# Optimization experiments

Hardware: AMD Instinct MI355X
Metric: run time of the kernel (lower is better)

Reference implementation:

```python
import jax, jax.numpy as jnp
import numpy as np


def _gat_layer(x, W, att_l, att_r, b, src, dst, num_nodes, heads, out_feat, concat):
    # x: [N, in], W: [in, H*F]
    xl = (x @ W).reshape(num_nodes, heads, out_feat)          # [N, H, F]
    a_l = jnp.sum(xl * att_l, axis=2)                          # [N, H]
    a_r = jnp.sum(xl * att_r, axis=2)                          # [N, H]
    # edge scores: alpha_j (source, att_l) + alpha_i (target, att_r)
    e = a_l[src] + a_r[dst]                                    # [E, H]
    e = jax.nn.leaky_relu(e, 0.2)
    # segment softmax over destination-node neighborhoods
    e_max = jax.ops.segment_max(e, dst, num_segments=num_nodes)
    e_exp = jnp.exp(e - e_max[dst])
    denom = jax.ops.segment_sum(e_exp, dst, num_segments=num_nodes)
    alpha = e_exp / (denom[dst] + 1e-16)                       # [E, H]
    # weighted gather + scatter-add aggregation
    msg = alpha[:, :, None] * xl[src]                          # [E, H, F]
    out = jax.ops.segment_sum(msg, dst, num_segments=num_nodes)  # [N, H, F]
    if concat:
        out = out.reshape(num_nodes, heads * out_feat)
    else:
        out = out.mean(axis=1)                                 # [N, F]
    return out + b


def setup_inputs() -> dict:
    key = jax.random.key(0)
    ks = jax.random.split(key, 8)
    N, E = 50000, 800000
    in_dim, hidden, out_dim, H = 128, 8, 64, 8
    x = jax.random.normal(ks[0], (N, in_dim), dtype=jnp.float32)
    edge_index = jax.random.randint(ks[1], (2, E), 0, N, dtype=jnp.int64)
    s = 0.1
    return {
        "x": x,
        "edge_index": edge_index,
        "W1": jax.random.normal(ks[2], (in_dim, hidden * H), dtype=jnp.float32) * s,
        "att_l1": jax.random.normal(ks[3], (1, H, hidden), dtype=jnp.float32) * s,
        "att_r1": jax.random.normal(ks[4], (1, H, hidden), dtype=jnp.float32) * s,
        "b1": jnp.zeros((hidden * H,), dtype=jnp.float32),
        "W2": jax.random.normal(ks[5], (hidden * H, out_dim * H), dtype=jnp.float32) * s,
        "att_l2": jax.random.normal(ks[6], (1, H, out_dim), dtype=jnp.float32) * s,
        "att_r2": jax.random.normal(ks[7], (1, H, out_dim), dtype=jnp.float32) * s,
        "b2": jnp.zeros((1, out_dim), dtype=jnp.float32),
    }


def reference(x, edge_index, W1, att_l1, att_r1, b1, W2, att_l2, att_r2, b2):
    N = x.shape[0]
    H = att_l1.shape[1]
    src, dst = edge_index[0], edge_index[1]
    h = _gat_layer(x, W1, att_l1, att_r1, b1, src, dst, N, H, att_l1.shape[2], concat=True)
    h = jax.nn.relu(h)
    out = _gat_layer(h, W2, att_l2, att_r2, b2, src, dst, N, H, att_l2.shape[2], concat=False)
    return out
```

## Files before the change

### kernel.cpp

```cpp
#include <hip/hip_runtime.h>
#include <stdint.h>

#define NT 256
#define CHUNK 4096
#define BSHIFT 8

typedef __attribute__((ext_vector_type(8))) short bf16x8;
typedef __attribute__((ext_vector_type(4))) float f32x4;

__device__ __forceinline__ float lrelu(float x) { return x > 0.f ? x : 0.2f * x; }

__device__ __forceinline__ float b2f(unsigned short u) {
  union { unsigned int i; float f; } v; v.i = ((unsigned int)u) << 16; return v.f;
}
__device__ __forceinline__ unsigned short f2b(float f) {
  unsigned int u = __float_as_uint(f);
  return (unsigned short)((u + 0x7fffu + ((u >> 16) & 1u)) >> 16);
}

__global__ void detect_kernel(const int* __restrict__ ei, int* __restrict__ flag, int twoE) {
  __shared__ int any;
  if (threadIdx.x == 0) any = 0;
  __syncthreads();
  int n = twoE < 4096 ? twoE : 4096;
  for (int i = threadIdx.x * 2 + 1; i < n; i += 2 * NT)
    if (ei[i] != 0) any = 1;
  __syncthreads();
  if (threadIdx.x == 0) *flag = any;
}

__global__ void cvtbin_kernel(const void* __restrict__ ei, const int* __restrict__ flag,
                              int* __restrict__ edges, int* __restrict__ blkcnt,
                              int E, int nblk, int nbk) {
  __shared__ int cnt[256];
  int b = blockIdx.x;
  for (int i = threadIdx.x; i < nbk; i += NT) cnt[i] = 0;
  __syncthreads();
  int beg = b * CHUNK;
  int end = beg + CHUNK < E ? beg + CHUNK : E;
  bool is32 = (*flag != 0);
  for (int i = beg + threadIdx.x; i < end; i += NT) {
    int s, d;
    if (is32) { s = ((const int*)ei)[i]; d = ((const int*)ei)[E + i]; }
    else      { s = (int)((const long long*)ei)[i]; d = (int)((const long long*)ei)[E + i]; }
    edges[i] = s;
    edges[E + i] = d;
    atomicAdd(&cnt[d >> BSHIFT], 1);
  }
  __syncthreads();
  for (int i = threadIdx.x; i < nbk; i += NT) blkcnt[i * nblk + b] = cnt[i];
}

__global__ void zero2_kernel(int* __restrict__ a, int* __restrict__ b, int n) {
  int i = blockIdx.x * NT + threadIdx.x;
  if (i < n) { a[i] = 0; b[i] = 0; }
}

__global__ void scan1_kernel(const int* __restrict__ in, int* __restrict__ bsum, int n) {
  __shared__ int sm[NT];
  int idx = blockIdx.x * NT + threadIdx.x;
  sm[threadIdx.x] = (idx < n) ? in[idx] : 0;
  __syncthreads();
  for (int s = NT / 2; s > 0; s >>= 1) {
    if (threadIdx.x < s) sm[threadIdx.x] += sm[threadIdx.x + s];
    __syncthreads();
  }
  if (threadIdx.x == 0) bsum[blockIdx.x] = sm[0];
}

__global__ void scan2_kernel(const int* __restrict__ bsum, int* __restrict__ boff, int SB) {
  __shared__ int sm[NT];
  int t = threadIdx.x;
  int v = (t < SB) ? bsum[t] : 0;
  sm[t] = v;
  __syncthreads();
  for (int s = 1; s < NT; s <<= 1) {
    int add = (t >= s) ? sm[t - s] : 0;
    __syncthreads();
    sm[t] += add;
    __syncthreads();
  }
  if (t < SB) boff[t] = sm[t] - v;
}

__global__ void scan3_kernel(const int* __restrict__ in, const int* __restrict__ boff,
                             int* __restrict__ out, int n) {
  __shared__ int sm[NT];
  int idx = blockIdx.x * NT + threadIdx.x;
  int v = (idx < n) ? in[idx] : 0;
  sm[threadIdx.x] = v;
  __syncthreads();
  for (int s = 1; s < NT; s <<= 1) {
    int add = (threadIdx.x >= s) ? sm[threadIdx.x - s] : 0;
    __syncthreads();
    sm[threadIdx.x] += add;
    __syncthreads();
  }
  if (idx <= n) out[idx] = boff[blockIdx.x] + sm[threadIdx.x] - v;
}

__global__ void binwrite_kernel(const int* __restrict__ src, const int* __restrict__ dst,
                                const int* __restrict__ base, long long* __restrict__ binned,
                                int E, int nblk, int nbk) {
  __shared__ int cnt[256];
  int b = blockIdx.x;
  for (int i = threadIdx.x; i < nbk; i += NT) cnt[i] = base[i * nblk + b];
  __syncthreads();
  int beg = b * CHUNK;
  int end = beg + CHUNK < E ? beg + CHUNK : E;
  for (int i = beg + threadIdx.x; i < end; i += NT) {
    int d = dst[i];
    int pos = atomicAdd(&cnt[d >> BSHIFT], 1);
    binned[pos] = ((long long)d << 32) | (unsigned int)src[i];
  }
}

__global__ void deghist_kernel(const long long* __restrict__ binned, int* __restrict__ deg, int E) {
  int e = blockIdx.x * NT + threadIdx.x;
  if (e < E) atomicAdd(&deg[(int)(binned[e] >> 32)], 1);
}

__global__ void scatter2_kernel(const long long* __restrict__ binned, const int* __restrict__ rowptr,
                                int* __restrict__ cursor, int* __restrict__ csr_src, int E) {
  int e = blockIdx.x * NT + threadIdx.x;
  if (e >= E) return;
  long long v = binned[e];
  int d = (int)(v >> 32);
  int s = (int)(v & 0xffffffffLL);
  int pos = rowptr[d] + atomicAdd(&cursor[d], 1);
  csr_src[pos] = s;
}

__global__ void foldB1_kernel(const float* __restrict__ W1, unsigned short* __restrict__ W1pack) {
  int idx = blockIdx.x * NT + threadIdx.x;
  if (idx >= 128 * 64) return;
  int j = idx & 7;
  int lane = (idx >> 3) & 63;
  int ctchunk = idx >> 9;
  int ct = ctchunk & 3;
  int chunk = ctchunk >> 2;
  int k = chunk * 32 + ((lane >> 4) << 3) + j;
  int col = ct * 16 + (lane & 15);
  W1pack[idx] = f2b(W1[k * 64 + col]);
}

__global__ void __launch_bounds__(NT)
gemm1_mfma_kernel(const float* __restrict__ x, const unsigned short* __restrict__ W1pack,
                  const float* __restrict__ attl, const float* __restrict__ attr,
                  unsigned short* __restrict__ xl1b, float* __restrict__ a1, int N) {
  int w = threadIdx.x >> 6;
  int lane = threadIdx.x & 63;
  int colb = lane & 15;
  int rgrp = lane >> 4;
  int row0w = blockIdx.x * 64 + w * 16;
  int arow = row0w + colb;
  if (arow >= N) arow = N - 1;
  const float* ap = x + (size_t)arow * 128 + (rgrp << 3);

  f32x4 acc[4];
#pragma unroll
  for (int ct = 0; ct < 4; ++ct) { acc[ct][0] = 0.f; acc[ct][1] = 0.f; acc[ct][2] = 0.f; acc[ct][3] = 0.f; }

#pragma unroll
  for (int chunk = 0; chunk < 4; ++chunk) {
    float4 v0 = *(const float4*)(ap + chunk * 32);
    float4 v1 = *(const float4*)(ap + chunk * 32 + 4);
    bf16x8 a;
    a[0] = (short)f2b(v0.x); a[1] = (short)f2b(v0.y);
    a[2] = (short)f2b(v0.z); a[3] = (short)f2b(v0.w);
    a[4] = (short)f2b(v1.x); a[5] = (short)f2b(v1.y);
    a[6] = (short)f2b(v1.z); a[7] = (short)f2b(v1.w);
    const unsigned short* bp = W1pack + ((size_t)chunk * 4 * 64 + lane) * 8;
#pragma unroll
    for (int ct = 0; ct < 4; ++ct) {
      bf16x8 b = *(const bf16x8*)(bp + (size_t)ct * 64 * 8);
      acc[ct] = __builtin_amdgcn_mfma_f32_16x16x32_bf16(a, b, acc[ct], 0, 0, 0);
    }
  }

#pragma unroll
  for (int ct = 0; ct < 4; ++ct) {
    float attlc = attl[ct * 16 + colb];
    float attrc = attr[ct * 16 + colb];
    int h = ct * 2 + (colb >> 3);
#pragma unroll
    for (int r = 0; r < 4; ++r) {
      int n = row0w + rgrp * 4 + r;
      float v = acc[ct][r];
      if (n < N) xl1b[(size_t)n * 64 + ct * 16 + colb] = f2b(v);
      float pl = v * attlc;
      float pr = v * attrc;
      pl += __shfl_xor(pl, 1, 64); pr += __shfl_xor(pr, 1, 64);
      pl += __shfl_xor(pl, 2, 64); pr += __shfl_xor(pr, 2, 64);
      pl += __shfl_xor(pl, 4, 64); pr += __shfl_xor(pr, 4, 64);
      if ((lane & 7) == 0 && n < N) {
        a1[n * 16 + h] = pl;
        a1[n * 16 + 8 + h] = pr;
      }
    }
  }
}

__global__ void foldw_kernel(const float* __restrict__ W2, const float* __restrict__ attl2,
                             const float* __restrict__ attr2, float* __restrict__ wl,
                             float* __restrict__ wr) {
  int t = threadIdx.x;
  int k = t >> 3, h = t & 7;
  float sl = 0.f, sr = 0.f;
  for (int f = 0; f < 64; ++f) {
    float w = W2[k * 512 + h * 64 + f];
    sl += w * attl2[h * 64 + f];
    sr += w * attr2[h * 64 + f];
  }
  wl[k * 8 + h] = sl;
  wr[k * 8 + h] = sr;
}

__global__ void foldB_kernel(const float* __restrict__ W2, unsigned short* __restrict__ Bpack) {
  int idx = blockIdx.x * NT + threadIdx.x;
  if (idx >= 512 * 64) return;
  int j = idx & 7;
  int lane = (idx >> 3) & 63;
  int ctchunk = idx >> 9;
  int ct = ctchunk & 3;
  int chunk = ctchunk >> 2;
  int hk = chunk * 32 + ((lane >> 4) << 3) + j;
  int h = hk >> 6, kk = hk & 63;
  int f = ct * 16 + (lane & 15);
  Bpack[idx] = f2b(W2[kk * 512 + h * 64 + f] * 0.125f);
}

__global__ void __launch_bounds__(NT)
node_aggr1_kernel(const int* __restrict__ rowptr, const int* __restrict__ csr_src,
                  const float* __restrict__ a1, const unsigned short* __restrict__ xl1b,
                  const float* __restrict__ b1, unsigned short* __restrict__ hrb, int N) {
  __shared__ float ps[4][64][8];
  __shared__ int ss[4][64];
  int w = threadIdx.x >> 6;
  int n = blockIdx.x * 4 + w;
  if (n >= N) return;
  int lane = threadIdx.x & 63;
  int hstage = lane & 7;
  int j8 = lane >> 3;
  int hown = lane >> 3;
  int base = rowptr[n];
  int deg = rowptr[n + 1] - base;

  float arh = a1[n * 16 + 8 + hstage];
  const unsigned short* xp = xl1b + lane;
  float acc = 0.f, dn = 0.f;

  for (int j0 = 0; j0 < deg; j0 += 64) {
    int cnt = deg - j0; if (cnt > 64) cnt = 64;
    if (lane < cnt) ss[w][lane] = csr_src[base + j0 + lane];
    asm volatile("s_waitcnt lgkmcnt(0)" ::: "memory");
    for (int jj = 0; jj < cnt; jj += 8) {
      int j = jj + j8;
      if (j < cnt) {
        int s = ss[w][j];
        float p = __expf(lrelu(a1[(unsigned)s * 16 + hstage] + arh));
        ps[w][j][hstage] = p;
      }
    }
    asm volatile("s_waitcnt lgkmcnt(0)" ::: "memory");
    int j = 0;
    for (; j + 4 <= cnt; j += 4) {
      int s0 = ss[w][j+0], s1 = ss[w][j+1], s2 = ss[w][j+2], s3 = ss[w][j+3];
      float p0 = ps[w][j+0][hown], p1 = ps[w][j+1][hown];
      float p2 = ps[w][j+2][hown], p3 = ps[w][j+3][hown];
      float v0 = b2f(xp[(unsigned)s0 * 64]), v1 = b2f(xp[(unsigned)s1 * 64]);
      float v2 = b2f(xp[(unsigned)s2 * 64]), v3 = b2f(xp[(unsigned)s3 * 64]);
      dn += (p0 + p1) + (p2 + p3);
      acc += p0 * v0 + p1 * v1 + p2 * v2 + p3 * v3;
    }
    for (; j < cnt; ++j) {
      int s = ss[w][j];
      float p = ps[w][j][hown];
      dn += p;
      acc += p * b2f(xp[(unsigned)s * 64]);
    }
  }
  acc = acc / (dn + 1e-16f);
  float hv = fmaxf(acc + b1[lane], 0.f);
  hrb[(size_t)n * 64 + lane] = f2b(hv);
}

#define A2N 256
__global__ void __launch_bounds__(NT)
a2dots_kernel(const unsigned short* __restrict__ hrb, const float* __restrict__ wl,
              const float* __restrict__ wr, float* __restrict__ a2, int N) {
  __shared__ unsigned short hs[A2N][65];
  __shared__ float wls[64 * 8], wrs[64 * 8];
  int tid = threadIdx.x;
  int n0 = blockIdx.x * A2N;
  for (int i = tid; i < 512; i += NT) { wls[i] = wl[i]; wrs[i] = wr[i]; }
  for (int i = tid; i < A2N * 8; i += NT) {
    int r = i >> 3, seg = i & 7;
    int n = n0 + r;
    uint4 v = make_uint4(0, 0, 0, 0);
    if (n < N) v = *(const uint4*)&hrb[(size_t)n * 64 + seg * 8];
    int c = seg * 8;
    hs[r][c + 0] = (unsigned short)(v.x);
    hs[r][c + 1] = (unsigned short)(v.x >> 16);
    hs[r][c + 2] = (unsigned short)(v.y);
    hs[r][c + 3] = (unsigned short)(v.y >> 16);
    hs[r][c + 4] = (unsigned short)(v.z);
    hs[r][c + 5] = (unsigned short)(v.z >> 16);
    hs[r][c + 6] = (unsigned short)(v.w);
    hs[r][c + 7] = (unsigned short)(v.w >> 16);
  }
  __syncthreads();
  float tl[8], tr[8];
#pragma unroll
  for (int h = 0; h < 8; ++h) { tl[h] = 0.f; tr[h] = 0.f; }
#pragma unroll 4
  for (int k = 0; k < 64; ++k) {
    float hv = b2f(hs[tid][k]);
    float4 l0 = *(const float4*)&wls[k * 8];
    float4 l1 = *(const float4*)&wls[k * 8 + 4];
    float4 r0 = *(const float4*)&wrs[k * 8];
    float4 r1 = *(const float4*)&wrs[k * 8 + 4];
    tl[0] += hv * l0.x; tl[1] += hv * l0.y; tl[2] += hv * l0.z; tl[3] += hv * l0.w;
    tl[4] += hv * l1.x; tl[5] += hv * l1.y; tl[6] += hv * l1.z; tl[7] += hv * l1.w;
    tr[0] += hv * r0.x; tr[1] += hv * r0.y; tr[2] += hv * r0.z; tr[3] += hv * r0.w;
    tr[4] += hv * r1.x; tr[5] += hv * r1.y; tr[6] += hv * r1.z; tr[7] += hv * r1.w;
  }
  int n = n0 + tid;
  if (n < N) {
    *(float4*)&a2[n * 16 + 0]  = make_float4(tl[0], tl[1], tl[2], tl[3]);
    *(float4*)&a2[n * 16 + 4]  = make_float4(tl[4], tl[5], tl[6], tl[7]);
    *(float4*)&a2[n * 16 + 8]  = make_float4(tr[0], tr[1], tr[2], tr[3]);
    *(float4*)&a2[n * 16 + 12] = make_float4(tr[4], tr[5], tr[6], tr[7]);
  }
}

__global__ void __launch_bounds__(NT)
node_aggr2_fused_kernel(const int* __restrict__ rowptr, const int* __restrict__ csr_src,
                        const float* __restrict__ a2, const unsigned short* __restrict__ hrb,
                        const unsigned short* __restrict__ Bpack, const float* __restrict__ b2,
                        float* __restrict__ out, int N) {
  __shared__ float ps[4][64][8];
  __shared__ int ss[4][64];
  __shared__ unsigned short gs[16][520];
  int w = threadIdx.x >> 6;
  int lane = threadIdx.x & 63;
  int hstage = lane & 7;
  int j8 = lane >> 3;

  for (int nr = 0; nr < 4; ++nr) {
    int row = w * 4 + nr;
    int n = blockIdx.x * 16 + row;
    if (n < N) {
      int base = rowptr[n];
      int deg = rowptr[n + 1] - base;
      float arh = a2[n * 16 + 8 + hstage];
      const unsigned short* hp = hrb + lane;
      float acc[8] = {0.f, 0.f, 0.f, 0.f, 0.f, 0.f, 0.f, 0.f};
      float dn_own = 0.f;

      for (int j0 = 0; j0 < deg; j0 += 64) {
        int cnt = deg - j0; if (cnt > 64) cnt = 64;
        if (lane < cnt) ss[w][lane] = csr_src[base + j0 + lane];
        asm volatile("s_waitcnt lgkmcnt(0)" ::: "memory");
        for (int jj = 0; jj < cnt; jj += 8) {
          int j = jj + j8;
          if (j < cnt) {
            int s = ss[w][j];
            float p = __expf(lrelu(a2[(unsigned)s * 16 + hstage] + arh));
            ps[w][j][hstage] = p;
          }
        }
        asm volatile("s_waitcnt lgkmcnt(0)" ::: "memory");
        for (int j = 0; j < cnt; ++j) {
          int s = ss[w][j];
          float hv = b2f(hp[(unsigned)s * 64]);
          float4 pa = *(const float4*)&ps[w][j][0];
          float4 pb = *(const float4*)&ps[w][j][4];
          dn_own += ps[w][j][hstage];
          acc[0] += pa.x * hv; acc[1] += pa.y * hv; acc[2] += pa.z * hv; acc[3] += pa.w * hv;
          acc[4] += pb.x * hv; acc[5] += pb.y * hv; acc[6] += pb.z * hv; acc[7] += pb.w * hv;
        }
      }
#pragma unroll
      for (int h = 0; h < 8; ++h) {
        float dnh = __shfl(dn_own, h, 64);
        float v = acc[h] * (1.f / (dnh + 1e-16f));
        gs[row][h * 64 + lane] = f2b(v);
      }
    } else {
#pragma unroll
      for (int h = 0; h < 8; ++h) gs[row][h * 64 + lane] = 0;
    }
  }
  __syncthreads();

  f32x4 acc4;
  {
    float bb = b2[w * 16 + (lane & 15)];
    acc4[0] = bb; acc4[1] = bb; acc4[2] = bb; acc4[3] = bb;
  }
  const unsigned short* ap = &gs[lane & 15][(lane >> 4) << 3];
#pragma unroll
  for (int chunk = 0; chunk < 16; ++chunk) {
    bf16x8 a = *(const bf16x8*)(ap + chunk * 32);
    bf16x8 b = *(const bf16x8*)(Bpack + ((size_t)(chunk * 4 + w) * 64 + lane) * 8);
    acc4 = __builtin_amdgcn_mfma_f32_16x16x32_bf16(a, b, acc4, 0, 0, 0);
  }
  int col = w * 16 + (lane & 15);
  int orow0 = (lane >> 4) << 2;
#pragma unroll
  for (int r = 0; r < 4; ++r) {
    int n = blockIdx.x * 16 + orow0 + r;
    if (n < N) out[(size_t)n * 64 + col] = acc4[r];
  }
}

extern "C" void kernel_launch(void* const* d_in, const int* in_sizes, int n_in,
                              void* d_out, int out_size, void* d_ws, size_t ws_size,
                              hipStream_t stream) {
  const float* x     = (const float*)d_in[0];
  const void*  ei    = d_in[1];
  const float* W1    = (const float*)d_in[2];
  const float* attl1 = (const float*)d_in[3];
  const float* attr1 = (const float*)d_in[4];
  const float* b1    = (const float*)d_in[5];
  const float* W2    = (const float*)d_in[6];
  const float* attl2 = (const float*)d_in[7];
  const float* attr2 = (const float*)d_in[8];
  const float* b2    = (const float*)d_in[9];
  float* out = (float*)d_out;

  int N = in_sizes[0] / 128;
  int E = in_sizes[1] / 2;

  int nblk = (E + CHUNK - 1) / CHUNK;
  int nbk  = (N + (1 << BSHIFT) - 1) >> BSHIFT;
  int L    = nbk * nblk;

  char* ws = (char*)d_ws;
  size_t off = 0;
  auto alloc = [&](size_t bytes) {
    char* p = ws + off;
    off += (bytes + 255) & ~size_t(255);
    return p;
  };
  int*            edges   = (int*)alloc((size_t)2 * E * 4);
  int*            flag    = (int*)alloc(256);
  int*            deg     = (int*)alloc((size_t)N * 4);
  int*            cursor  = (int*)alloc((size_t)N * 4);
  int*            rowptr  = (int*)alloc((size_t)(N + 1) * 4);
  int*            bsum    = (int*)alloc(1024);
  int*            boff    = (int*)alloc(1024);
  int*            blkcnt  = (int*)alloc((size_t)L * 4);
  int*            basebuf = (int*)alloc((size_t)(L + 1) * 4);
  int*            bsum2   = (int*)alloc(1024);
  int*            boff2   = (int*)alloc(1024);
  long long*      binned  = (long long*)alloc((size_t)E * 8);
  int*            csr_src = (int*)alloc((size_t)E * 4);
  unsigned short* xl1b    = (unsigned short*)alloc((size_t)N * 64 * 2);
  float*          a1      = (float*)alloc((size_t)N * 16 * 4);
  unsigned short* hrb     = (unsigned short*)alloc((size_t)N * 64 * 2);
  float*          a2      = (float*)alloc((size_t)N * 16 * 4);
  float*          wl      = (float*)alloc(64 * 8 * 4);
  float*          wr      = (float*)alloc(64 * 8 * 4);
  unsigned short* Bpack   = (unsigned short*)alloc(512 * 64 * 2);
  unsigned short* W1pack  = (unsigned short*)alloc(128 * 64 * 2);
  (void)ws_size;

  const int* srcp = edges;
  const int* dstp = edges + E;
  int SB  = (N + 1 + NT - 1) / NT;
  int SBL = (L + 1 + NT - 1) / NT;

  detect_kernel<<<1, NT, 0, stream>>>((const int*)ei, flag, 2 * E);
  zero2_kernel<<<(N + NT - 1) / NT, NT, 0, stream>>>(deg, cursor, N);

  cvtbin_kernel<<<nblk, NT, 0, stream>>>(ei, flag, edges, blkcnt, E, nblk, nbk);
  scan1_kernel<<<SBL, NT, 0, stream>>>(blkcnt, bsum2, L);
  scan2_kernel<<<1, NT, 0, stream>>>(bsum2, boff2, SBL);
  scan3_kernel<<<SBL, NT, 0, stream>>>(blkcnt, boff2, basebuf, L);
  binwrite_kernel<<<nblk, NT, 0, stream>>>(srcp, dstp, basebuf, binned, E, nblk, nbk);

  deghist_kernel<<<(E + NT - 1) / NT, NT, 0, stream>>>(binned, deg, E);
  scan1_kernel<<<SB, NT, 0, stream>>>(deg, bsum, N);
  scan2_kernel<<<1, NT, 0, stream>>>(bsum, boff, SB);
  scan3_kernel<<<SB, NT, 0, stream>>>(deg, boff, rowptr, N);

  scatter2_kernel<<<(E + NT - 1) / NT, NT, 0, stream>>>(binned, rowptr, cursor, csr_src, E);

  foldB1_kernel<<<(128 * 64 + NT - 1) / NT, NT, 0, stream>>>(W1, W1pack);
  gemm1_mfma_kernel<<<(N + 63) / 64, NT, 0, stream>>>(x, W1pack, attl1, attr1, xl1b, a1, N);
  foldw_kernel<<<1, 512, 0, stream>>>(W2, attl2, attr2, wl, wr);
  foldB_kernel<<<(512 * 64 + NT - 1) / NT, NT, 0, stream>>>(W2, Bpack);

  node_aggr1_kernel<<<(N + 3) / 4, NT, 0, stream>>>(rowptr, csr_src, a1, xl1b, b1, hrb, N);

  a2dots_kernel<<<(N + A2N - 1) / A2N, NT, 0, stream>>>(hrb, wl, wr, a2, N);

  node_aggr2_fused_kernel<<<(N + 15) / 16, NT, 0, stream>>>(rowptr, csr_src, a2, hrb, Bpack, b2, out, N);
}
```

Baseline: 252.6 us.

## Assign one wave per node in layer-2 aggregation and merge setup kernels

Layer-2 aggregation now uses 1024-thread blocks where each of 16 waves gathers one destination node, instead of 4 waves each looping over 4 nodes. Only 4 waves then run the MFMA projection. The denominator is reduced with shuffles instead of an extra shared-memory read. Degree counting is folded into the edge conversion kernel, and the three weight-folding kernels are merged into one launch to cut launch count. The costs are larger shared-memory use per block and global atomics on degrees in unsorted edge order.

```diff
diff --git a/kernel.cpp b/kernel.cpp
--- a/kernel.cpp
+++ b/kernel.cpp
@@ -29,9 +29,14 @@
   if (threadIdx.x == 0) *flag = any;
 }
 
+__global__ void zero2_kernel(int* __restrict__ a, int* __restrict__ b, int n) {
+  int i = blockIdx.x * NT + threadIdx.x;
+  if (i < n) { a[i] = 0; b[i] = 0; }
+}
+
 __global__ void cvtbin_kernel(const void* __restrict__ ei, const int* __restrict__ flag,
                               int* __restrict__ edges, int* __restrict__ blkcnt,
-                              int E, int nblk, int nbk) {
+                              int* __restrict__ deg, int E, int nblk, int nbk) {
   __shared__ int cnt[256];
   int b = blockIdx.x;
   for (int i = threadIdx.x; i < nbk; i += NT) cnt[i] = 0;
@@ -46,14 +51,10 @@
     edges[i] = s;
     edges[E + i] = d;
     atomicAdd(&cnt[d >> BSHIFT], 1);
+    atomicAdd(&deg[d], 1);
   }
   __syncthreads();
   for (int i = threadIdx.x; i < nbk; i += NT) blkcnt[i * nblk + b] = cnt[i];
-}
-
-__global__ void zero2_kernel(int* __restrict__ a, int* __restrict__ b, int n) {
-  int i = blockIdx.x * NT + threadIdx.x;
-  if (i < n) { a[i] = 0; b[i] = 0; }
 }
 
 __global__ void scan1_kernel(const int* __restrict__ in, int* __restrict__ bsum, int n) {
@@ -113,11 +114,6 @@
     int pos = atomicAdd(&cnt[d >> BSHIFT], 1);
     binned[pos] = ((long long)d << 32) | (unsigned int)src[i];
   }
-}
-
-__global__ void deghist_kernel(const long long* __restrict__ binned, int* __restrict__ deg, int E) {
-  int e = blockIdx.x * NT + threadIdx.x;
-  if (e < E) atomicAdd(&deg[(int)(binned[e] >> 32)], 1);
 }
 
 __global__ void scatter2_kernel(const long long* __restrict__ binned, const int* __restrict__ rowptr,
@@ -131,17 +127,45 @@
   csr_src[pos] = s;
 }
 
-__global__ void foldB1_kernel(const float* __restrict__ W1, unsigned short* __restrict__ W1pack) {
-  int idx = blockIdx.x * NT + threadIdx.x;
-  if (idx >= 128 * 64) return;
-  int j = idx & 7;
-  int lane = (idx >> 3) & 63;
-  int ctchunk = idx >> 9;
-  int ct = ctchunk & 3;
-  int chunk = ctchunk >> 2;
-  int k = chunk * 32 + ((lane >> 4) << 3) + j;
-  int col = ct * 16 + (lane & 15);
-  W1pack[idx] = f2b(W1[k * 64 + col]);
+__global__ void foldall_kernel(const float* __restrict__ W1, const float* __restrict__ W2,
+                               const float* __restrict__ attl2, const float* __restrict__ attr2,
+                               unsigned short* __restrict__ W1pack, unsigned short* __restrict__ Bpack,
+                               float* __restrict__ wl, float* __restrict__ wr) {
+  int b = blockIdx.x;
+  if (b < 128) {
+    int idx = b * NT + threadIdx.x;
+    int j = idx & 7;
+    int lane = (idx >> 3) & 63;
+    int ctchunk = idx >> 9;
+    int ct = ctchunk & 3;
+    int chunk = ctchunk >> 2;
+    int hk = chunk * 32 + ((lane >> 4) << 3) + j;
+    int h = hk >> 6, kk = hk & 63;
+    int f = ct * 16 + (lane & 15);
+    Bpack[idx] = f2b(W2[kk * 512 + h * 64 + f] * 0.125f);
+  } else if (b < 160) {
+    int idx = (b - 128) * NT + threadIdx.x;
+    int j = idx & 7;
+    int lane = (idx >> 3) & 63;
+    int ctchunk = idx >> 9;
+    int ct = ctchunk & 3;
+    int chunk = ctchunk >> 2;
+    int k = chunk * 32 + ((lane >> 4) << 3) + j;
+    int col = ct * 16 + (lane & 15);
+    W1pack[idx] = f2b(W1[k * 64 + col]);
+  } else {
+    for (int t = threadIdx.x; t < 512; t += NT) {
+      int k = t >> 3, h = t & 7;
+      float sl = 0.f, sr = 0.f;
+      for (int f = 0; f < 64; ++f) {
+        float w = W2[k * 512 + h * 64 + f];
+        sl += w * attl2[h * 64 + f];
+        sr += w * attr2[h * 64 + f];
+      }
+      wl[k * 8 + h] = sl;
+      wr[k * 8 + h] = sr;
+    }
+  }
 }
 
 __global__ void __launch_bounds__(NT)
@@ -199,35 +223,6 @@
       }
     }
   }
-}
-
-__global__ void foldw_kernel(const float* __restrict__ W2, const float* __restrict__ attl2,
-                             const float* __restrict__ attr2, float* __restrict__ wl,
-                             float* __restrict__ wr) {
-  int t = threadIdx.x;
-  int k = t >> 3, h = t & 7;
-  float sl = 0.f, sr = 0.f;
-  for (int f = 0; f < 64; ++f) {
-    float w = W2[k * 512 + h * 64 + f];
-    sl += w * attl2[h * 64 + f];
-    sr += w * attr2[h * 64 + f];
-  }
-  wl[k * 8 + h] = sl;
-  wr[k * 8 + h] = sr;
-}
-
-__global__ void foldB_kernel(const float* __restrict__ W2, unsigned short* __restrict__ Bpack) {
-  int idx = blockIdx.x * NT + threadIdx.x;
-  if (idx >= 512 * 64) return;
-  int j = idx & 7;
-  int lane = (idx >> 3) & 63;
-  int ctchunk = idx >> 9;
-  int ct = ctchunk & 3;
-  int chunk = ctchunk >> 2;
-  int hk = chunk * 32 + ((lane >> 4) << 3) + j;
-  int h = hk >> 6, kk = hk & 63;
-  int f = ct * 16 + (lane & 15);
-  Bpack[idx] = f2b(W2[kk * 512 + h * 64 + f] * 0.125f);
 }
 
 __global__ void __launch_bounds__(NT)
@@ -334,84 +329,86 @@
   }
 }
 
-__global__ void __launch_bounds__(NT)
-node_aggr2_fused_kernel(const int* __restrict__ rowptr, const int* __restrict__ csr_src,
-                        const float* __restrict__ a2, const unsigned short* __restrict__ hrb,
-                        const unsigned short* __restrict__ Bpack, const float* __restrict__ b2,
-                        float* __restrict__ out, int N) {
-  __shared__ float ps[4][64][8];
-  __shared__ int ss[4][64];
+__global__ void __launch_bounds__(1024)
+node_aggr2_mfma_kernel(const int* __restrict__ rowptr, const int* __restrict__ csr_src,
+                       const float* __restrict__ a2, const unsigned short* __restrict__ hrb,
+                       const unsigned short* __restrict__ Bpack, const float* __restrict__ b2,
+                       float* __restrict__ out, int N) {
+  __shared__ float ps[16][64][8];
+  __shared__ int ss[16][64];
   __shared__ unsigned short gs[16][520];
   int w = threadIdx.x >> 6;
   int lane = threadIdx.x & 63;
   int hstage = lane & 7;
   int j8 = lane >> 3;
-
-  for (int nr = 0; nr < 4; ++nr) {
-    int row = w * 4 + nr;
-    int n = blockIdx.x * 16 + row;
-    if (n < N) {
-      int base = rowptr[n];
-      int deg = rowptr[n + 1] - base;
-      float arh = a2[n * 16 + 8 + hstage];
-      const unsigned short* hp = hrb + lane;
-      float acc[8] = {0.f, 0.f, 0.f, 0.f, 0.f, 0.f, 0.f, 0.f};
-      float dn_own = 0.f;
-
-      for (int j0 = 0; j0 < deg; j0 += 64) {
-        int cnt = deg - j0; if (cnt > 64) cnt = 64;
-        if (lane < cnt) ss[w][lane] = csr_src[base + j0 + lane];
-        asm volatile("s_waitcnt lgkmcnt(0)" ::: "memory");
-        for (int jj = 0; jj < cnt; jj += 8) {
-          int j = jj + j8;
-          if (j < cnt) {
-            int s = ss[w][j];
-            float p = __expf(lrelu(a2[(unsigned)s * 16 + hstage] + arh));
-            ps[w][j][hstage] = p;
-          }
-        }
-        asm volatile("s_waitcnt lgkmcnt(0)" ::: "memory");
-        for (int j = 0; j < cnt; ++j) {
+  int n = blockIdx.x * 16 + w;
+
+  if (n < N) {
+    int base = rowptr[n];
+    int deg = rowptr[n + 1] - base;
+    float arh = a2[n * 16 + 8 + hstage];
+    const unsigned short* hp = hrb + lane;
+    float acc[8] = {0.f, 0.f, 0.f, 0.f, 0.f, 0.f, 0.f, 0.f};
+    float dnst = 0.f;
+
+    for (int j0 = 0; j0 < deg; j0 += 64) {
+      int cnt = deg - j0; if (cnt > 64) cnt = 64;
+      if (lane < cnt) ss[w][lane] = csr_src[base + j0 + lane];
+      asm volatile("s_waitcnt lgkmcnt(0)" ::: "memory");
+      for (int jj = 0; jj < cnt; jj += 8) {
+        int j = jj + j8;
+        if (j < cnt) {
           int s = ss[w][j];
-          float hv = b2f(hp[(unsigned)s * 64]);
-          float4 pa = *(const float4*)&ps[w][j][0];
-          float4 pb = *(const float4*)&ps[w][j][4];
-          dn_own += ps[w][j][hstage];
-          acc[0] += pa.x * hv; acc[1] += pa.y * hv; acc[2] += pa.z * hv; acc[3] += pa.w * hv;
-          acc[4] += pb.x * hv; acc[5] += pb.y * hv; acc[6] += pb.z * hv; acc[7] += pb.w * hv;
+          float p = __expf(lrelu(a2[(unsigned)s * 16 + hstage] + arh));
+          dnst += p;
+          ps[w][j][hstage] = p;
         }
       }
-#pragma unroll
-      for (int h = 0; h < 8; ++h) {
-        float dnh = __shfl(dn_own, h, 64);
-        float v = acc[h] * (1.f / (dnh + 1e-16f));
-        gs[row][h * 64 + lane] = f2b(v);
+      asm volatile("s_waitcnt lgkmcnt(0)" ::: "memory");
+      for (int j = 0; j < cnt; ++j) {
+        int s = ss[w][j];
+        float hv = b2f(hp[(unsigned)s * 64]);
+        float4 pa = *(const float4*)&ps[w][j][0];
+        float4 pb = *(const float4*)&ps[w][j][4];
+        acc[0] += pa.x * hv; acc[1] += pa.y * hv; acc[2] += pa.z * hv; acc[3] += pa.w * hv;
+        acc[4] += pb.x * hv; acc[5] += pb.y * hv; acc[6] += pb.z * hv; acc[7] += pb.w * hv;
       }
-    } else {
-#pragma unroll
-      for (int h = 0; h < 8; ++h) gs[row][h * 64 + lane] = 0;
-    }
-  }
-  __syncthreads();
-
-  f32x4 acc4;
-  {
-    float bb = b2[w * 16 + (lane & 15)];
-    acc4[0] = bb; acc4[1] = bb; acc4[2] = bb; acc4[3] = bb;
-  }
-  const unsigned short* ap = &gs[lane & 15][(lane >> 4) << 3];
-#pragma unroll
-  for (int chunk = 0; chunk < 16; ++chunk) {
-    bf16x8 a = *(const bf16x8*)(ap + chunk * 32);
-    bf16x8 b = *(const bf16x8*)(Bpack + ((size_t)(chunk * 4 + w) * 64 + lane) * 8);
-    acc4 = __builtin_amdgcn_mfma_f32_16x16x32_bf16(a, b, acc4, 0, 0, 0);
-  }
-  int col = w * 16 + (lane & 15);
-  int orow0 = (lane >> 4) << 2;
-#pragma unroll
-  for (int r = 0; r < 4; ++r) {
-    int n = blockIdx.x * 16 + orow0 + r;
-    if (n < N) out[(size_t)n * 64 + col] = acc4[r];
+    }
+    dnst += __shfl_xor(dnst, 8, 64);
+    dnst += __shfl_xor(dnst, 16, 64);
+    dnst += __shfl_xor(dnst, 32, 64);
+#pragma unroll
+    for (int h = 0; h < 8; ++h) {
+      float dnh = __shfl(dnst, h, 64);
+      float v = acc[h] * (1.f / (dnh + 1e-16f));
+      gs[w][h * 64 + lane] = f2b(v);
+    }
+  } else {
+#pragma unroll
+    for (int h = 0; h < 8; ++h) gs[w][h * 64 + lane] = 0;
+  }
+  __syncthreads();
+
+  if (w < 4) {
+    f32x4 acc4;
+    {
+      float bb = b2[w * 16 + (lane & 15)];
+      acc4[0] = bb; acc4[1] = bb; acc4[2] = bb; acc4[3] = bb;
+    }
+    const unsigned short* ap = &gs[lane & 15][(lane >> 4) << 3];
+#pragma unroll
+    for (int chunk = 0; chunk < 16; ++chunk) {
+      bf16x8 a = *(const bf16x8*)(ap + chunk * 32);
+      bf16x8 b = *(const bf16x8*)(Bpack + ((size_t)(chunk * 4 + w) * 64 + lane) * 8);
+      acc4 = __builtin_amdgcn_mfma_f32_16x16x32_bf16(a, b, acc4, 0, 0, 0);
+    }
+    int col = w * 16 + (lane & 15);
+    int orow0 = (lane >> 4) << 2;
+#pragma unroll
+    for (int r = 0; r < 4; ++r) {
+      int nn = blockIdx.x * 16 + orow0 + r;
+      if (nn < N) out[(size_t)nn * 64 + col] = acc4[r];
+    }
   }
 }
 
@@ -475,27 +472,24 @@
   detect_kernel<<<1, NT, 0, stream>>>((const int*)ei, flag, 2 * E);
   zero2_kernel<<<(N + NT - 1) / NT, NT, 0, stream>>>(deg, cursor, N);
 
-  cvtbin_kernel<<<nblk, NT, 0, stream>>>(ei, flag, edges, blkcnt, E, nblk, nbk);
+  cvtbin_kernel<<<nblk, NT, 0, stream>>>(ei, flag, edges, blkcnt, deg, E, nblk, nbk);
   scan1_kernel<<<SBL, NT, 0, stream>>>(blkcnt, bsum2, L);
   scan2_kernel<<<1, NT, 0, stream>>>(bsum2, boff2, SBL);
   scan3_kernel<<<SBL, NT, 0, stream>>>(blkcnt, boff2, basebuf, L);
   binwrite_kernel<<<nblk, NT, 0, stream>>>(srcp, dstp, basebuf, binned, E, nblk, nbk);
 
-  deghist_kernel<<<(E + NT - 1) / NT, NT, 0, stream>>>(binned, deg, E);
   scan1_kernel<<<SB, NT, 0, stream>>>(deg, bsum, N);
   scan2_kernel<<<1, NT, 0, stream>>>(bsum, boff, SB);
   scan3_kernel<<<SB, NT, 0, stream>>>(deg, boff, rowptr, N);
 
   scatter2_kernel<<<(E + NT - 1) / NT, NT, 0, stream>>>(binned, rowptr, cursor, csr_src, E);
 
-  foldB1_kernel<<<(128 * 64 + NT - 1) / NT, NT, 0, stream>>>(W1, W1pack);
+  foldall_kernel<<<161, NT, 0, stream>>>(W1, W2, attl2, attr2, W1pack, Bpack, wl, wr);
   gemm1_mfma_kernel<<<(N + 63) / 64, NT, 0, stream>>>(x, W1pack, attl1, attr1, xl1b, a1, N);
-  foldw_kernel<<<1, 512, 0, stream>>>(W2, attl2, attr2, wl, wr);
-  foldB_kernel<<<(512 * 64 + NT - 1) / NT, NT, 0, stream>>>(W2, Bpack);
 
   node_aggr1_kernel<<<(N + 3) / 4, NT, 0, stream>>>(rowptr, csr_src, a1, xl1b, b1, hrb, N);
 
   a2dots_kernel<<<(N + A2N - 1) / A2N, NT, 0, stream>>>(hrb, wl, wr, a2, N);
 
-  node_aggr2_fused_kernel<<<(N + 15) / 16, NT, 0, stream>>>(rowptr, csr_src, a2, hrb, Bpack, b2, out, N);
-}
+  node_aggr2_mfma_kernel<<<(N + 15) / 16, 1024, 0, stream>>>(rowptr, csr_src, a2, hrb, Bpack, b2, out, N);
+}
```

Result: faster. 244.1 us (-3.4%).
